# Optimization experiments

Measured on AMD Instinct MI355X. Metric: run time of the kernel, lower is better.

The kernel has to match this reference:

```python
import jax, jax.numpy as jnp
import numpy as np

NG, NU, NI, H = 5000, 100000, 20000, 128
E_UG, E_UI, E_GI = 300000, 600000, 200000


def setup_inputs() -> dict:
    key = jax.random.key(0)
    ks = jax.random.split(key, 20)
    s = 0.05  # weight scale for numeric stability
    inp = {
        'x_group': jnp.arange(NG, dtype=jnp.int64) if False else jnp.arange(NG),
        'x_user': jnp.arange(NU),
        'x_item': jnp.arange(NI),
        'emb_group': jax.random.normal(ks[0], (NG, H), jnp.float32) * s,
        'emb_user': jax.random.normal(ks[1], (NU, H), jnp.float32) * s,
        'emb_item': jax.random.normal(ks[2], (NI, H), jnp.float32) * s,
        'W1l': jax.random.normal(ks[3], (6, H, H), jnp.float32) * s,
        'W1r': jax.random.normal(ks[4], (6, H, H), jnp.float32) * s,
        'b1': jax.random.normal(ks[5], (6, H), jnp.float32) * s,
        'W2l': jax.random.normal(ks[6], (6, H, H), jnp.float32) * s,
        'W2r': jax.random.normal(ks[7], (6, H, H), jnp.float32) * s,
        'b2': jax.random.normal(ks[8], (6, H), jnp.float32) * s,
        'pred_W': jax.random.normal(ks[9], (H, NI), jnp.float32) * s,
        'pred_b': jax.random.normal(ks[10], (NI,), jnp.float32) * s,
        'ug_src': jax.random.randint(ks[11], (E_UG,), 0, NU),
        'ug_dst': jax.random.randint(ks[12], (E_UG,), 0, NG),
        'ui_src': jax.random.randint(ks[13], (E_UI,), 0, NU),
        'ui_dst': jax.random.randint(ks[14], (E_UI,), 0, NI),
        'gi_src': jax.random.randint(ks[15], (E_GI,), 0, NG),
        'gi_dst': jax.random.randint(ks[16], (E_GI,), 0, NI),
    }
    return inp


def _seg_mean(x, src, dst, n_dst):
    # gather neighbor features [E, H], scatter-sum to dst, divide by in-degree
    s = jax.ops.segment_sum(x[src], dst, num_segments=n_dst)
    cnt = jax.ops.segment_sum(jnp.ones(dst.shape[0], x.dtype), dst, num_segments=n_dst)
    return s / jnp.clip(cnt, 1.0)[:, None]


def _hetero_sage_layer(hg, hu, hi, Wl, Wr, b,
                       ug_src, ug_dst, ui_src, ui_dst, gi_src, gi_dst):
    # edge-type order: 0 u2g, 1 g2u, 2 u2i, 3 i2u, 4 g2i, 5 i2g
    ng, nu, ni = hg.shape[0], hu.shape[0], hi.shape[0]
    og = (_seg_mean(hu, ug_src, ug_dst, ng) @ Wl[0] + hg @ Wr[0] + b[0]
          + _seg_mean(hi, gi_dst, gi_src, ng) @ Wl[5] + hg @ Wr[5] + b[5])
    ou = (_seg_mean(hg, ug_dst, ug_src, nu) @ Wl[1] + hu @ Wr[1] + b[1]
          + _seg_mean(hi, ui_dst, ui_src, nu) @ Wl[3] + hu @ Wr[3] + b[3])
    oi = (_seg_mean(hu, ui_src, ui_dst, ni) @ Wl[2] + hi @ Wr[2] + b[2]
          + _seg_mean(hg, gi_src, gi_dst, ni) @ Wl[4] + hi @ Wr[4] + b[4])
    return og, ou, oi


def reference(x_group, x_user, x_item, emb_group, emb_user, emb_item,
              W1l, W1r, b1, W2l, W2r, b2, pred_W, pred_b,
              ug_src, ug_dst, ui_src, ui_dst, gi_src, gi_dst):
    # embedding lookup; group embeddings are zeroed in BaseGR.forward
    hg = emb_group[x_group] * 0.0
    hu = emb_user[x_user]
    hi = emb_item[x_item]
    og, ou, oi = _hetero_sage_layer(hg, hu, hi, W1l, W1r, b1,
                                    ug_src, ug_dst, ui_src, ui_dst, gi_src, gi_dst)
    hg, hu, hi = jax.nn.relu(og), jax.nn.relu(ou), jax.nn.relu(oi)
    og, ou, oi = _hetero_sage_layer(hg, hu, hi, W2l, W2r, b2,
                                    ug_src, ug_dst, ui_src, ui_dst, gi_src, gi_dst)
    rep_group = jax.nn.relu(og)
    # eval-mode output: group-level item scores [NG, NI]
    return rep_group @ pred_W + pred_b
```

## Files before the change

### kernel.cpp

```cpp
#include <hip/hip_runtime.h>

typedef __bf16 bf16x8 __attribute__((ext_vector_type(8)));
typedef __bf16 bf16x4 __attribute__((ext_vector_type(4)));
typedef __bf16 bf16x2 __attribute__((ext_vector_type(2)));
typedef float  f32x4  __attribute__((ext_vector_type(4)));

#define NG 5000
#define NU 100000
#define NI 20000
#define H  128
#define EUG 300000
#define EUI 600000
#define EGI 200000
#define ETOT (EUG + EGI + EUI + EUI)
#define NN  (2 * NG + NU + NI)

#define B_EMBU  0UL
#define B_EMBI  25600000UL
#define B_AGGU  30720000UL
#define B_AGGI  56320000UL
#define B_AGGG1 61440000UL
#define B_AGGG2 62720000UL
#define B_HG1   64000000UL
#define B_GU    65280000UL
#define B_GI    66560000UL
#define B_REP   67840000UL
#define B_BC    69120000UL
#define B_PWT   69122048UL
#define B_WT    74242048UL
#define B_CNT   74536960UL
#define B_OFFS  75056960UL
#define B_CUR   75576976UL
#define B_EIDX  76096976UL
#define B_EIT   82897024UL


#define SCAN_CHUNK 2048
#define NCHUNK 64

#define NB_PREP 10
#define NB_TP   626
#define NB_CVU  12500
#define NB_CVI  2500
#define NB_HIST 6641
#define NB_P1   (NB_PREP + NB_TP + NB_CVU + NB_CVI + NB_HIST)

#define NBU 782
#define NBI 157
#define NBG 40

__device__ __forceinline__ int swz(int row, int k) {
  return ((((k >> 3) ^ (row & 15)) << 3) | (k & 7));
}
__device__ __forceinline__ int cswz(int row, int col) {
  return col ^ (((row >> 2) & 1) << 4);
}

__device__ void prep_dev(const float* __restrict__ W1l, const float* __restrict__ W1r,
                         const float* __restrict__ W2l, const float* __restrict__ W2r,
                         const float* __restrict__ b1, const float* __restrict__ b2,
                         __bf16* __restrict__ WT, float* __restrict__ bc, int b, int tid) {
  if (b < 9) {
    const float* Wa; const float* Wb = nullptr;
    switch (b) {
      case 0: Wa = W1r + 1 * 16384; Wb = W1r + 3 * 16384; break;
      case 1: Wa = W1l + 3 * 16384; break;
      case 2: Wa = W1l + 2 * 16384; break;
      case 3: Wa = W1r + 2 * 16384; Wb = W1r + 4 * 16384; break;
      case 4: Wa = W1l + 0 * 16384; break;
      case 5: Wa = W1l + 5 * 16384; break;
      case 6: Wa = W2r + 0 * 16384; Wb = W2r + 5 * 16384; break;
      case 7: Wa = W2l + 0 * 16384; break;
      default: Wa = W2l + 5 * 16384; break;
    }
    __bf16* dst = WT + b * 16384;
    for (int idx = tid; idx < 16384; idx += 256) {
      int k = idx >> 7, c = idx & 127;
      float v = Wa[idx];
      if (Wb) v += Wb[idx];
      dst[c * 128 + k] = (__bf16)v;
    }
  } else {
    if (tid < 128) {
      bc[tid]       = b1[128 + tid]     + b1[3 * 128 + tid];
      bc[128 + tid] = b1[2 * 128 + tid] + b1[4 * 128 + tid];
      bc[256 + tid] = b1[tid]           + b1[5 * 128 + tid];
      bc[384 + tid] = b2[tid]           + b2[5 * 128 + tid];
    }
  }
}

__device__ void transpose_dev(const float* __restrict__ pw, __bf16* __restrict__ pwt,
                              int bx, int by, int tid, float (*t)[65]) {
  int i0 = bx * 64, k0 = by * 64;
  for (int idx = tid; idx < 64 * 16; idx += 256) {
    int kk = idx >> 4, c4 = (idx & 15) << 2;
    int ib = i0 + c4;
    float x0 = 0.f, x1 = 0.f, x2 = 0.f, x3 = 0.f;
    const float* src = pw + (size_t)(k0 + kk) * NI + ib;
    if (ib + 3 < NI) {
      const float4 v = *(const float4*)src;
      x0 = v.x; x1 = v.y; x2 = v.z; x3 = v.w;
    } else {
      if (ib + 0 < NI) x0 = src[0];
      if (ib + 1 < NI) x1 = src[1];
      if (ib + 2 < NI) x2 = src[2];
      if (ib + 3 < NI) x3 = src[3];
    }
    t[kk][c4 + 0] = x0; t[kk][c4 + 1] = x1; t[kk][c4 + 2] = x2; t[kk][c4 + 3] = x3;
  }
  __syncthreads();
  for (int idx = tid; idx < 64 * 16; idx += 256) {
    int ii = idx >> 4, k4 = (idx & 15) << 2;
    int gi = i0 + ii;
    if (gi < NI) {
      bf16x4 o;
      o[0] = (__bf16)t[k4 + 0][ii]; o[1] = (__bf16)t[k4 + 1][ii];
      o[2] = (__bf16)t[k4 + 2][ii]; o[3] = (__bf16)t[k4 + 3][ii];
      *(bf16x4*)(pwt + (size_t)gi * 128 + k0 + k4) = o;
    }
  }
}

__device__ void cvt_dev(const float* __restrict__ src, __bf16* __restrict__ dst,
                        int b, int tid, int n4) {
  int i = b * 256 + tid;
  if (i < n4) {
    float4 v = ((const float4*)src)[i];
    bf16x4 o;
    o[0] = (__bf16)v.x; o[1] = (__bf16)v.y; o[2] = (__bf16)v.z; o[3] = (__bf16)v.w;
    ((bf16x4*)dst)[i] = o;
  }
}

__device__ void hist_dev(const int* __restrict__ ug_dst, const int* __restrict__ gi_src,
                         const int* __restrict__ ui_src, const int* __restrict__ ui_dst,
                         int* __restrict__ cnt, int b, int tid) {
  int i = b * 256 + tid;
  int key, base;
  if (i < EUG)                       { key = ug_dst[i];                   base = 0; }
  else if (i < EUG + EGI)            { key = gi_src[i - EUG];             base = NG; }
  else if (i < EUG + EGI + EUI)      { key = ui_src[i - EUG - EGI];       base = 2 * NG; }
  else if (i < ETOT)                 { key = ui_dst[i - EUG - EGI - EUI]; base = 2 * NG + NU; }
  else return;
  atomicAdd(&cnt[base + key], 1);
}

__device__ void gemm_core(const __bf16* __restrict__ A0, const __bf16* __restrict__ B0,
                          const __bf16* __restrict__ A1, const __bf16* __restrict__ B1,
                          const __bf16* __restrict__ A2, const __bf16* __restrict__ B2,
                          const __bf16* __restrict__ Dadd, const float* __restrict__ bias,
                          float* __restrict__ Cf, __bf16* __restrict__ Cb,
                          int N, int NC, int nterms, int relu,
                          int rowblk, int colblk, char* smem_raw) {
  __bf16* sA = (__bf16*)smem_raw;
  __bf16* sB = sA + 128 * 128;
  float* sC = (float*)smem_raw;
  int tid = threadIdx.x;
  int rowbase = rowblk * 128, colbase = colblk * 128;
  int wid = tid >> 6, lane = tid & 63;
  int qrow = (wid >> 1) << 6, qcol = (wid & 1) << 6;
  int lrow = lane & 15, quad = lane >> 4;

  f32x4 acc[4][4];
#pragma unroll
  for (int mi = 0; mi < 4; ++mi)
#pragma unroll
    for (int ni = 0; ni < 4; ++ni) acc[mi][ni] = (f32x4){0.f, 0.f, 0.f, 0.f};

  const __bf16* As[3] = {A0, A1, A2};
  const __bf16* Bs[3] = {B0, B1, B2};

  for (int t = 0; t < nterms; ++t) {
    __syncthreads();
    const __bf16* A = As[t];
    for (int idx = tid; idx < 2048; idx += 256) {
      int row = idx >> 4, c8 = (idx & 15) << 3;
      int grow = rowbase + row;
      bf16x8 v;
      if (grow < N) v = *(const bf16x8*)(A + (size_t)grow * 128 + c8);
      else { for (int u = 0; u < 8; ++u) v[u] = (__bf16)0.f; }
      *(bf16x8*)&sA[row * 128 + swz(row, c8)] = v;
    }
    const __bf16* B = Bs[t];
    for (int idx = tid; idx < 2048; idx += 256) {
      int n = idx >> 4, c8 = (idx & 15) << 3;
      int gcol = colbase + n;
      bf16x8 v;
      if (gcol < NC) v = *(const bf16x8*)(B + (size_t)gcol * 128 + c8);
      else { for (int u = 0; u < 8; ++u) v[u] = (__bf16)0.f; }
      *(bf16x8*)&sB[n * 128 + swz(n, c8)] = v;
    }
    __syncthreads();
#pragma unroll
    for (int kb = 0; kb < 4; ++kb) {
      int k0 = kb * 32 + quad * 8;
      bf16x8 af[4], bfr[4];
#pragma unroll
      for (int mi = 0; mi < 4; ++mi) {
        int r = qrow + mi * 16 + lrow;
        af[mi] = *(const bf16x8*)&sA[r * 128 + swz(r, k0)];
      }
#pragma unroll
      for (int ni = 0; ni < 4; ++ni) {
        int r = qcol + ni * 16 + lrow;
        bfr[ni] = *(const bf16x8*)&sB[r * 128 + swz(r, k0)];
      }
#pragma unroll
      for (int mi = 0; mi < 4; ++mi)
#pragma unroll
        for (int ni = 0; ni < 4; ++ni)
          acc[mi][ni] = __builtin_amdgcn_mfma_f32_16x16x32_bf16(af[mi], bfr[ni], acc[mi][ni], 0, 0, 0);
    }
  }

  __syncthreads();
#pragma unroll
  for (int mi = 0; mi < 4; ++mi) {
#pragma unroll
    for (int ni = 0; ni < 4; ++ni) {
      int col = qcol + ni * 16 + lrow;
#pragma unroll
      for (int r = 0; r < 4; ++r) {
        int row = qrow + mi * 16 + quad * 4 + r;
        sC[row * 128 + cswz(row, col)] = acc[mi][ni][r];
      }
    }
  }
  __syncthreads();
  for (int idx = tid; idx < 4096; idx += 256) {
    int row = idx >> 5, c4 = (idx & 31) << 2;
    int grow = rowbase + row, gcol = colbase + c4;
    if (grow >= N) continue;
    f32x4 v = *(const f32x4*)&sC[row * 128 + cswz(row, c4)];
    if (gcol + 3 < NC) {
      if (bias) {
        f32x4 bv = *(const f32x4*)&bias[gcol];
        v += bv;
      }
      if (Dadd) {
        bf16x4 dv = *(const bf16x4*)(Dadd + (size_t)grow * 128 + gcol);
        v[0] += (float)dv[0]; v[1] += (float)dv[1];
        v[2] += (float)dv[2]; v[3] += (float)dv[3];
      }
      if (relu) {
#pragma unroll
        for (int u = 0; u < 4; ++u) v[u] = fmaxf(v[u], 0.f);
      }
      if (Cb) {
        bf16x4 o;
        o[0] = (__bf16)v[0]; o[1] = (__bf16)v[1]; o[2] = (__bf16)v[2]; o[3] = (__bf16)v[3];
        *(bf16x4*)(Cb + (size_t)grow * NC + gcol) = o;
      } else {
        __builtin_nontemporal_store(v, (f32x4*)(Cf + (size_t)grow * NC + gcol));
      }
    } else {
#pragma unroll
      for (int u = 0; u < 4; ++u) {
        if (gcol + u < NC) {
          float x = v[u] + (bias ? bias[gcol + u] : 0.f);
          if (Dadd) x += (float)Dadd[(size_t)grow * 128 + gcol + u];
          if (relu) x = fmaxf(x, 0.f);
          if (Cb) Cb[(size_t)grow * NC + gcol + u] = (__bf16)x;
          else    Cf[(size_t)grow * NC + gcol + u] = x;
        }
      }
    }
  }
}

__device__ void seg_dev(const __bf16* __restrict__ feat, const int* __restrict__ offs,
                        const int* __restrict__ eidx, __bf16* __restrict__ out,
                        int node, int orow, int lane) {
  int s = offs[node], e = offs[node + 1];
  float a0 = 0.f, a1 = 0.f;
  int j = s;
  for (; j + 4 <= e; j += 4) {
    int i0 = eidx[j], i1 = eidx[j + 1], i2 = eidx[j + 2], i3 = eidx[j + 3];
    bf16x2 v0 = *(const bf16x2*)(feat + (size_t)i0 * 128 + lane * 2);
    bf16x2 v1 = *(const bf16x2*)(feat + (size_t)i1 * 128 + lane * 2);
    bf16x2 v2 = *(const bf16x2*)(feat + (size_t)i2 * 128 + lane * 2);
    bf16x2 v3 = *(const bf16x2*)(feat + (size_t)i3 * 128 + lane * 2);
    a0 += (float)v0[0] + (float)v1[0] + (float)v2[0] + (float)v3[0];
    a1 += (float)v0[1] + (float)v1[1] + (float)v2[1] + (float)v3[1];
  }
  if (j + 2 <= e) {
    int i0 = eidx[j], i1 = eidx[j + 1];
    bf16x2 v0 = *(const bf16x2*)(feat + (size_t)i0 * 128 + lane * 2);
    bf16x2 v1 = *(const bf16x2*)(feat + (size_t)i1 * 128 + lane * 2);
    a0 += (float)v0[0] + (float)v1[0];
    a1 += (float)v0[1] + (float)v1[1];
    j += 2;
  }
  if (j < e) {
    int i0 = eidx[j];
    bf16x2 v0 = *(const bf16x2*)(feat + (size_t)i0 * 128 + lane * 2);
    a0 += (float)v0[0]; a1 += (float)v0[1];
  }
  float inv = (e > s) ? (1.f / (float)(e - s)) : 0.f;
  bf16x2 o;
  o[0] = (__bf16)(a0 * inv); o[1] = (__bf16)(a1 * inv);
  *(bf16x2*)(out + (size_t)orow * 128 + lane * 2) = o;
}

__global__ __launch_bounds__(256)
void phase1(const float* __restrict__ W1l, const float* __restrict__ W1r,
            const float* __restrict__ W2l, const float* __restrict__ W2r,
            const float* __restrict__ b1, const float* __restrict__ b2,
            const float* __restrict__ predW,
            const float* __restrict__ emb_user, const float* __restrict__ emb_item,
            const int* __restrict__ ug_dst, const int* __restrict__ gi_src,
            const int* __restrict__ ui_src, const int* __restrict__ ui_dst,
            char* __restrict__ ws) {
  __shared__ float tbuf[64][65];
  __bf16* WT = (__bf16*)(ws + B_WT);
  float* bc  = (float*)(ws + B_BC);
  __bf16* pwt = (__bf16*)(ws + B_PWT);
  __bf16* embU = (__bf16*)(ws + B_EMBU);
  __bf16* embI = (__bf16*)(ws + B_EMBI);
  int* cnt = (int*)(ws + B_CNT);
  int b = blockIdx.x, tid = threadIdx.x;
  if (b < NB_PREP) { prep_dev(W1l, W1r, W2l, W2r, b1, b2, WT, bc, b, tid); return; }
  b -= NB_PREP;
  if (b < NB_TP) { transpose_dev(predW, pwt, b % 313, b / 313, tid, tbuf); return; }
  b -= NB_TP;
  if (b < NB_CVU) { cvt_dev(emb_user, embU, b, tid, NU * 32); return; }
  b -= NB_CVU;
  if (b < NB_CVI) { cvt_dev(emb_item, embI, b, tid, NI * 32); return; }
  b -= NB_CVI;
  hist_dev(ug_dst, gi_src, ui_src, ui_dst, cnt, b, tid);
}

__global__ __launch_bounds__(256)
void scan_k1(const int* __restrict__ cnt, int* __restrict__ chunksum) {
  __shared__ int ws4[4];
  int b = blockIdx.x, tid = threadIdx.x, lane = tid & 63, w = tid >> 6;
  int base = b * SCAN_CHUNK + tid * 8;
  int s = 0;
#pragma unroll
  for (int j = 0; j < 8; ++j) { int i = base + j; if (i < NN) s += cnt[i]; }
#pragma unroll
  for (int d = 1; d < 64; d <<= 1) s += __shfl_xor(s, d, 64);
  if (lane == 0) ws4[w] = s;
  __syncthreads();
  if (tid == 0) chunksum[b] = ws4[0] + ws4[1] + ws4[2] + ws4[3];
}

__global__ __launch_bounds__(256)
void scan2_gemm0(char* __restrict__ ws) {
  __shared__ char smem[65536];
  int b = blockIdx.x, tid = threadIdx.x;
  if (b < NCHUNK) {
    int* shi = (int*)smem;
    const int* cnt = (const int*)(ws + B_CNT);
    const int* chunksum = (const int*)(ws + B_AGGU);
    int* offs = (int*)(ws + B_OFFS);
    int* cur  = (int*)(ws + B_CUR);
    int lane = tid & 63, w = tid >> 6;
    if (w == 0) {
      int v = chunksum[lane];
      int incl = v;
#pragma unroll
      for (int d = 1; d < 64; d <<= 1) { int t = __shfl_up(incl, d, 64); if (lane >= d) incl += t; }
      if (lane == b) shi[4] = incl - v;
    }
    int base = b * SCAN_CHUNK + tid * 8;
    int x[8]; int s = 0;
#pragma unroll
    for (int j = 0; j < 8; ++j) { int i = base + j; x[j] = (i < NN) ? cnt[i] : 0; s += x[j]; }
    int incl = s;
#pragma unroll
    for (int d = 1; d < 64; d <<= 1) { int t = __shfl_up(incl, d, 64); if (lane >= d) incl += t; }
    if (lane == 63) shi[w] = incl;
    __syncthreads();
    int wpre = 0;
    for (int ww = 0; ww < w; ++ww) wpre += shi[ww];
    int excl = shi[4] + wpre + incl - s;
#pragma unroll
    for (int j = 0; j < 8; ++j) {
      int i = base + j;
      if (i < NN) { offs[i] = excl; cur[i] = excl; }
      excl += x[j];
      if (i == NN - 1) offs[NN] = excl;
    }
  } else {
    const __bf16* embI = (const __bf16*)(ws + B_EMBI);
    const __bf16* WT   = (const __bf16*)(ws + B_WT);
    __bf16* eit = (__bf16*)(ws + B_EIT);
    gemm_core(embI, WT + 1 * 16384, nullptr, nullptr, nullptr, nullptr,
              nullptr, nullptr, nullptr, eit, NI, 128, 1, 0, b - NCHUNK, 0, smem);
  }
}

__global__ __launch_bounds__(256)
void fill_all(const int* __restrict__ ug_src, const int* __restrict__ ug_dst,
              const int* __restrict__ gi_src, const int* __restrict__ gi_dst,
              const int* __restrict__ ui_src, const int* __restrict__ ui_dst,
              int* __restrict__ cur, int* __restrict__ eidx) {
  int i = blockIdx.x * 256 + threadIdx.x;
  int key, base, payload;
  if (i < EUG)                  { key = ug_dst[i];       base = 0;            payload = ug_src[i]; }
  else if (i < EUG + EGI)       { int j = i - EUG;       key = gi_src[j]; base = NG;          payload = gi_dst[j]; }
  else if (i < EUG + EGI + EUI) { int j = i - EUG - EGI; key = ui_src[j]; base = 2 * NG;      payload = ui_dst[j]; }
  else if (i < ETOT)            { int j = i - EUG - EGI - EUI; key = ui_dst[j]; base = 2 * NG + NU; payload = ui_src[j]; }
  else return;
  int pos = atomicAdd(&cur[base + key], 1);
  eidx[pos] = payload;
}

__global__ __launch_bounds__(256)
void seg1(char* __restrict__ ws) {
  int w = threadIdx.x >> 6, lane = threadIdx.x & 63;
  int node = blockIdx.x * 4 + w;
  if (node >= NN) return;
  const int* offs = (const int*)(ws + B_OFFS);
  const int* eidx = (const int*)(ws + B_EIDX);
  const __bf16* feat; __bf16* out; int orow;
  if (node < NG)               { feat = (const __bf16*)(ws + B_EMBU); out = (__bf16*)(ws + B_AGGG1); orow = node; }
  else if (node < 2 * NG)      { feat = (const __bf16*)(ws + B_EMBI); out = (__bf16*)(ws + B_AGGG2); orow = node - NG; }
  else if (node < 2 * NG + NU) { feat = (const __bf16*)(ws + B_EIT);  out = (__bf16*)(ws + B_AGGU);  orow = node - 2 * NG; }
  else                         { feat = (const __bf16*)(ws + B_EMBU); out = (__bf16*)(ws + B_AGGI);  orow = node - 2 * NG - NU; }
  seg_dev(feat, offs, eidx, out, node, orow, lane);
}

__global__ __launch_bounds__(256)
void gemm1(char* __restrict__ ws) {
  __shared__ char smem[65536];
  const __bf16* WT = (const __bf16*)(ws + B_WT);
  const float* bc  = (const float*)(ws + B_BC);
  int b = blockIdx.x;
  if (b < NBU) {
    __bf16* aggU = (__bf16*)(ws + B_AGGU);
    gemm_core((const __bf16*)(ws + B_EMBU), WT + 0 * 16384,
              nullptr, nullptr, nullptr, nullptr,
              aggU, bc + 0, nullptr, aggU, NU, 128, 1, 1, b, 0, smem);
  } else if (b < NBU + NBI) {
    __bf16* aggI = (__bf16*)(ws + B_AGGI);
    gemm_core(aggI, WT + 2 * 16384,
              (const __bf16*)(ws + B_EMBI), WT + 3 * 16384, nullptr, nullptr,
              nullptr, bc + 128, nullptr, aggI, NI, 128, 2, 1, b - NBU, 0, smem);
  } else {
    gemm_core((const __bf16*)(ws + B_AGGG1), WT + 4 * 16384,
              (const __bf16*)(ws + B_AGGG2), WT + 5 * 16384, nullptr, nullptr,
              nullptr, bc + 256, nullptr, (__bf16*)(ws + B_HG1), NG, 128, 2, 1,
              b - NBU - NBI, 0, smem);
  }
}

__global__ __launch_bounds__(256)
void seg2(char* __restrict__ ws) {
  int w = threadIdx.x >> 6, lane = threadIdx.x & 63;
  int node = blockIdx.x * 4 + w;
  if (node >= 2 * NG) return;
  const int* offs = (const int*)(ws + B_OFFS);
  const int* eidx = (const int*)(ws + B_EIDX);
  const __bf16* feat; __bf16* out; int orow;
  if (node < NG) { feat = (const __bf16*)(ws + B_AGGU); out = (__bf16*)(ws + B_GU); orow = node; }
  else           { feat = (const __bf16*)(ws + B_AGGI); out = (__bf16*)(ws + B_GI); orow = node - NG; }
  seg_dev(feat, offs, eidx, out, node, orow, lane);
}

__global__ __launch_bounds__(256)
void gemm2(char* __restrict__ ws) {
  __shared__ char smem[65536];
  const __bf16* WT = (const __bf16*)(ws + B_WT);
  const float* bc  = (const float*)(ws + B_BC);
  gemm_core((const __bf16*)(ws + B_GU),  WT + 7 * 16384,
            (const __bf16*)(ws + B_HG1), WT + 6 * 16384,
            (const __bf16*)(ws + B_GI),  WT + 8 * 16384,
            nullptr, bc + 384, nullptr, (__bf16*)(ws + B_REP), NG, 128, 3, 1,
            blockIdx.x, 0, smem);
}

__global__ __launch_bounds__(256)
void gemmF(char* __restrict__ ws, const float* __restrict__ predb, float* __restrict__ out) {
  __shared__ char smem[65536];
  gemm_core((const __bf16*)(ws + B_REP), (const __bf16*)(ws + B_PWT),
            nullptr, nullptr, nullptr, nullptr,
            nullptr, predb, out, nullptr, NG, NI, 1, 0,
            blockIdx.x, blockIdx.y, smem);
}

extern "C" void kernel_launch(void* const* d_in, const int* in_sizes, int n_in,
                              void* d_out, int out_size, void* d_ws, size_t ws_size,
                              hipStream_t stream) {
  const float* emb_user = (const float*)d_in[4];
  const float* emb_item = (const float*)d_in[5];
  const float* W1l = (const float*)d_in[6];
  const float* W1r = (const float*)d_in[7];
  const float* b1  = (const float*)d_in[8];
  const float* W2l = (const float*)d_in[9];
  const float* W2r = (const float*)d_in[10];
  const float* b2  = (const float*)d_in[11];
  const float* predW = (const float*)d_in[12];
  const float* predb = (const float*)d_in[13];
  const int* ug_src = (const int*)d_in[14];
  const int* ug_dst = (const int*)d_in[15];
  const int* ui_src = (const int*)d_in[16];
  const int* ui_dst = (const int*)d_in[17];
  const int* gi_src = (const int*)d_in[18];
  const int* gi_dst = (const int*)d_in[19];

  char* ws = (char*)d_ws;
  int* cnt  = (int*)(ws + B_CNT);
  int* cur  = (int*)(ws + B_CUR);
  int* eidx = (int*)(ws + B_EIDX);
  int* chunksum = (int*)(ws + B_AGGU);

  hipMemsetAsync(cnt, 0, NN * sizeof(int), stream);

  phase1<<<NB_P1, 256, 0, stream>>>(W1l, W1r, W2l, W2r, b1, b2, predW,
                                    emb_user, emb_item,
                                    ug_dst, gi_src, ui_src, ui_dst, ws);
  scan_k1<<<NCHUNK, 256, 0, stream>>>(cnt, chunksum);
  scan2_gemm0<<<NCHUNK + NBI, 256, 0, stream>>>(ws);
  fill_all<<<(ETOT + 255) / 256, 256, 0, stream>>>(ug_src, ug_dst, gi_src, gi_dst,
                                                   ui_src, ui_dst, cur, eidx);
  seg1<<<(NN + 3) / 4, 256, 0, stream>>>(ws);
  gemm1<<<NBU + NBI + NBG, 256, 0, stream>>>(ws);
  seg2<<<(2 * NG + 3) / 4, 256, 0, stream>>>(ws);
  gemm2<<<NBG, 256, 0, stream>>>(ws);
  gemmF<<<dim3(NBG, NBI), 256, 0, stream>>>(ws, predb, (float*)d_out);
}
```

Measured before the change: 924.5 us.

## Merge pipeline into two persistent kernels with software grid barriers

Replaces nine kernel launches with two persistent kernels (768 and 384 blocks) that loop over virtual blocks and synchronise between phases with an atomic generation-counter grid barrier. The algebra is also reordered: the item-to-user transform is no longer precomputed before aggregation but applied afterwards in the user GEMM as a second term, which drops the EIT buffer and the Dadd epilogue. The segment-mean routine is changed so each half-wave handles alternate edges with 4-wide loads and a shuffle reduce. This removes launch gaps and the pre-GEMM, but the barriers assume all blocks are co-resident, give up on a timeout, and persistent grids may balance work less well.

```diff
diff --git a/kernel.cpp b/kernel.cpp
--- a/kernel.cpp
+++ b/kernel.cpp
@@ -28,11 +28,11 @@
 #define B_BC    69120000UL
 #define B_PWT   69122048UL
 #define B_WT    74242048UL
-#define B_CNT   74536960UL
-#define B_OFFS  75056960UL
-#define B_CUR   75576976UL
-#define B_EIDX  76096976UL
-#define B_EIT   82897024UL
+#define B_BAR   74536960UL
+#define B_CNT   74537088UL
+#define B_OFFS  75057088UL
+#define B_CUR   75577104UL
+#define B_EIDX  76097104UL
 
 
 #define SCAN_CHUNK 2048
@@ -48,6 +48,29 @@
 #define NBU 782
 #define NBI 157
 #define NBG 40
+
+#define GRID_B 768
+#define GRID_C 384
+
+__device__ __forceinline__ void gbar(int* bar, int nb) {
+  __syncthreads();
+  if (threadIdx.x == 0) {
+    int* cnt = bar;
+    int* gen = bar + 16;
+    int g = __hip_atomic_load(gen, __ATOMIC_RELAXED, __HIP_MEMORY_SCOPE_AGENT);
+    if (__hip_atomic_fetch_add(cnt, 1, __ATOMIC_ACQ_REL, __HIP_MEMORY_SCOPE_AGENT) == nb - 1) {
+      __hip_atomic_store(cnt, 0, __ATOMIC_RELAXED, __HIP_MEMORY_SCOPE_AGENT);
+      __hip_atomic_store(gen, g + 1, __ATOMIC_RELEASE, __HIP_MEMORY_SCOPE_AGENT);
+    } else {
+      int spins = 0;
+      while (__hip_atomic_load(gen, __ATOMIC_ACQUIRE, __HIP_MEMORY_SCOPE_AGENT) == g) {
+        __builtin_amdgcn_s_sleep(8);
+        if (++spins > (1 << 16)) break;
+      }
+    }
+  }
+  __syncthreads();
+}
 
 __device__ __forceinline__ int swz(int row, int k) {
   return ((((k >> 3) ^ (row & 15)) << 3) | (k & 7));
@@ -120,6 +143,7 @@
       *(bf16x4*)(pwt + (size_t)gi * 128 + k0 + k4) = o;
     }
   }
+  __syncthreads();
 }
 
 __device__ void cvt_dev(const float* __restrict__ src, __bf16* __restrict__ dst,
@@ -149,7 +173,7 @@
 __device__ void gemm_core(const __bf16* __restrict__ A0, const __bf16* __restrict__ B0,
                           const __bf16* __restrict__ A1, const __bf16* __restrict__ B1,
                           const __bf16* __restrict__ A2, const __bf16* __restrict__ B2,
-                          const __bf16* __restrict__ Dadd, const float* __restrict__ bias,
+                          const float* __restrict__ bias,
                           float* __restrict__ Cf, __bf16* __restrict__ Cb,
                           int N, int NC, int nterms, int relu,
                           int rowblk, int colblk, char* smem_raw) {
@@ -238,11 +262,6 @@
         f32x4 bv = *(const f32x4*)&bias[gcol];
         v += bv;
       }
-      if (Dadd) {
-        bf16x4 dv = *(const bf16x4*)(Dadd + (size_t)grow * 128 + gcol);
-        v[0] += (float)dv[0]; v[1] += (float)dv[1];
-        v[2] += (float)dv[2]; v[3] += (float)dv[3];
-      }
       if (relu) {
 #pragma unroll
         for (int u = 0; u < 4; ++u) v[u] = fmaxf(v[u], 0.f);
@@ -259,7 +278,6 @@
       for (int u = 0; u < 4; ++u) {
         if (gcol + u < NC) {
           float x = v[u] + (bias ? bias[gcol + u] : 0.f);
-          if (Dadd) x += (float)Dadd[(size_t)grow * 128 + gcol + u];
           if (relu) x = fmaxf(x, 0.f);
           if (Cb) Cb[(size_t)grow * NC + gcol + u] = (__bf16)x;
           else    Cf[(size_t)grow * NC + gcol + u] = x;
@@ -267,104 +285,110 @@
       }
     }
   }
+  __syncthreads();
 }
 
 __device__ void seg_dev(const __bf16* __restrict__ feat, const int* __restrict__ offs,
                         const int* __restrict__ eidx, __bf16* __restrict__ out,
                         int node, int orow, int lane) {
   int s = offs[node], e = offs[node + 1];
-  float a0 = 0.f, a1 = 0.f;
-  int j = s;
-  for (; j + 4 <= e; j += 4) {
-    int i0 = eidx[j], i1 = eidx[j + 1], i2 = eidx[j + 2], i3 = eidx[j + 3];
-    bf16x2 v0 = *(const bf16x2*)(feat + (size_t)i0 * 128 + lane * 2);
-    bf16x2 v1 = *(const bf16x2*)(feat + (size_t)i1 * 128 + lane * 2);
-    bf16x2 v2 = *(const bf16x2*)(feat + (size_t)i2 * 128 + lane * 2);
-    bf16x2 v3 = *(const bf16x2*)(feat + (size_t)i3 * 128 + lane * 2);
-    a0 += (float)v0[0] + (float)v1[0] + (float)v2[0] + (float)v3[0];
-    a1 += (float)v0[1] + (float)v1[1] + (float)v2[1] + (float)v3[1];
-  }
-  if (j + 2 <= e) {
-    int i0 = eidx[j], i1 = eidx[j + 1];
-    bf16x2 v0 = *(const bf16x2*)(feat + (size_t)i0 * 128 + lane * 2);
-    bf16x2 v1 = *(const bf16x2*)(feat + (size_t)i1 * 128 + lane * 2);
+  int half = lane >> 5;
+  int l4 = (lane & 31) << 2;
+  float a0 = 0.f, a1 = 0.f, a2 = 0.f, a3 = 0.f;
+  int j = s + half;
+  for (; j + 2 < e; j += 4) {
+    int r0 = eidx[j], r1 = eidx[j + 2];
+    bf16x4 v0 = *(const bf16x4*)(feat + (size_t)r0 * 128 + l4);
+    bf16x4 v1 = *(const bf16x4*)(feat + (size_t)r1 * 128 + l4);
     a0 += (float)v0[0] + (float)v1[0];
     a1 += (float)v0[1] + (float)v1[1];
-    j += 2;
+    a2 += (float)v0[2] + (float)v1[2];
+    a3 += (float)v0[3] + (float)v1[3];
   }
   if (j < e) {
-    int i0 = eidx[j];
-    bf16x2 v0 = *(const bf16x2*)(feat + (size_t)i0 * 128 + lane * 2);
-    a0 += (float)v0[0]; a1 += (float)v0[1];
-  }
-  float inv = (e > s) ? (1.f / (float)(e - s)) : 0.f;
-  bf16x2 o;
-  o[0] = (__bf16)(a0 * inv); o[1] = (__bf16)(a1 * inv);
-  *(bf16x2*)(out + (size_t)orow * 128 + lane * 2) = o;
-}
-
-__global__ __launch_bounds__(256)
-void phase1(const float* __restrict__ W1l, const float* __restrict__ W1r,
-            const float* __restrict__ W2l, const float* __restrict__ W2r,
-            const float* __restrict__ b1, const float* __restrict__ b2,
-            const float* __restrict__ predW,
-            const float* __restrict__ emb_user, const float* __restrict__ emb_item,
-            const int* __restrict__ ug_dst, const int* __restrict__ gi_src,
-            const int* __restrict__ ui_src, const int* __restrict__ ui_dst,
-            char* __restrict__ ws) {
+    int r0 = eidx[j];
+    bf16x4 v0 = *(const bf16x4*)(feat + (size_t)r0 * 128 + l4);
+    a0 += (float)v0[0]; a1 += (float)v0[1]; a2 += (float)v0[2]; a3 += (float)v0[3];
+  }
+  a0 += __shfl_xor(a0, 32, 64);
+  a1 += __shfl_xor(a1, 32, 64);
+  a2 += __shfl_xor(a2, 32, 64);
+  a3 += __shfl_xor(a3, 32, 64);
+  if (half == 0) {
+    float inv = (e > s) ? (1.f / (float)(e - s)) : 0.f;
+    bf16x4 o;
+    o[0] = (__bf16)(a0 * inv); o[1] = (__bf16)(a1 * inv);
+    o[2] = (__bf16)(a2 * inv); o[3] = (__bf16)(a3 * inv);
+    *(bf16x4*)(out + (size_t)orow * 128 + l4) = o;
+  }
+}
+
+__global__ __launch_bounds__(256, 4)
+void coopB(const float* __restrict__ W1l, const float* __restrict__ W1r,
+           const float* __restrict__ W2l, const float* __restrict__ W2r,
+           const float* __restrict__ b1, const float* __restrict__ b2,
+           const float* __restrict__ predW,
+           const float* __restrict__ emb_user, const float* __restrict__ emb_item,
+           const int* __restrict__ ug_src, const int* __restrict__ ug_dst,
+           const int* __restrict__ ui_src, const int* __restrict__ ui_dst,
+           const int* __restrict__ gi_src, const int* __restrict__ gi_dst,
+           char* __restrict__ ws) {
   __shared__ float tbuf[64][65];
+  __shared__ int shi[8];
+  int tid = threadIdx.x;
+  int nb = gridDim.x;
+  int* bar = (int*)(ws + B_BAR);
+
   __bf16* WT = (__bf16*)(ws + B_WT);
   float* bc  = (float*)(ws + B_BC);
   __bf16* pwt = (__bf16*)(ws + B_PWT);
   __bf16* embU = (__bf16*)(ws + B_EMBU);
   __bf16* embI = (__bf16*)(ws + B_EMBI);
-  int* cnt = (int*)(ws + B_CNT);
-  int b = blockIdx.x, tid = threadIdx.x;
-  if (b < NB_PREP) { prep_dev(W1l, W1r, W2l, W2r, b1, b2, WT, bc, b, tid); return; }
-  b -= NB_PREP;
-  if (b < NB_TP) { transpose_dev(predW, pwt, b % 313, b / 313, tid, tbuf); return; }
-  b -= NB_TP;
-  if (b < NB_CVU) { cvt_dev(emb_user, embU, b, tid, NU * 32); return; }
-  b -= NB_CVU;
-  if (b < NB_CVI) { cvt_dev(emb_item, embI, b, tid, NI * 32); return; }
-  b -= NB_CVI;
-  hist_dev(ug_dst, gi_src, ui_src, ui_dst, cnt, b, tid);
-}
-
-__global__ __launch_bounds__(256)
-void scan_k1(const int* __restrict__ cnt, int* __restrict__ chunksum) {
-  __shared__ int ws4[4];
-  int b = blockIdx.x, tid = threadIdx.x, lane = tid & 63, w = tid >> 6;
-  int base = b * SCAN_CHUNK + tid * 8;
-  int s = 0;
-#pragma unroll
-  for (int j = 0; j < 8; ++j) { int i = base + j; if (i < NN) s += cnt[i]; }
-#pragma unroll
-  for (int d = 1; d < 64; d <<= 1) s += __shfl_xor(s, d, 64);
-  if (lane == 0) ws4[w] = s;
-  __syncthreads();
-  if (tid == 0) chunksum[b] = ws4[0] + ws4[1] + ws4[2] + ws4[3];
-}
-
-__global__ __launch_bounds__(256)
-void scan2_gemm0(char* __restrict__ ws) {
-  __shared__ char smem[65536];
-  int b = blockIdx.x, tid = threadIdx.x;
-  if (b < NCHUNK) {
-    int* shi = (int*)smem;
-    const int* cnt = (const int*)(ws + B_CNT);
-    const int* chunksum = (const int*)(ws + B_AGGU);
-    int* offs = (int*)(ws + B_OFFS);
-    int* cur  = (int*)(ws + B_CUR);
+  int* cnt  = (int*)(ws + B_CNT);
+  int* offs = (int*)(ws + B_OFFS);
+  int* cur  = (int*)(ws + B_CUR);
+  int* eidx = (int*)(ws + B_EIDX);
+  int* chunksum = (int*)(ws + B_AGGU);
+
+  for (int vb = blockIdx.x; vb < NB_P1; vb += nb) {
+    int b = vb;
+    if (b < NB_PREP) { prep_dev(W1l, W1r, W2l, W2r, b1, b2, WT, bc, b, tid); continue; }
+    b -= NB_PREP;
+    if (b < NB_TP) { transpose_dev(predW, pwt, b % 313, b / 313, tid, tbuf); continue; }
+    b -= NB_TP;
+    if (b < NB_CVU) { cvt_dev(emb_user, embU, b, tid, NU * 32); continue; }
+    b -= NB_CVU;
+    if (b < NB_CVI) { cvt_dev(emb_item, embI, b, tid, NI * 32); continue; }
+    b -= NB_CVI;
+    hist_dev(ug_dst, gi_src, ui_src, ui_dst, cnt, b, tid);
+  }
+  gbar(bar, nb);
+
+  for (int vb = blockIdx.x; vb < NCHUNK; vb += nb) {
+    int lane = tid & 63, w = tid >> 6;
+    int base = vb * SCAN_CHUNK + tid * 8;
+    int s = 0;
+#pragma unroll
+    for (int j = 0; j < 8; ++j) { int i = base + j; if (i < NN) s += cnt[i]; }
+#pragma unroll
+    for (int d = 1; d < 64; d <<= 1) s += __shfl_xor(s, d, 64);
+    if (lane == 0) shi[w] = s;
+    __syncthreads();
+    if (tid == 0) chunksum[vb] = shi[0] + shi[1] + shi[2] + shi[3];
+    __syncthreads();
+  }
+  gbar(bar, nb);
+
+  for (int vb = blockIdx.x; vb < NCHUNK; vb += nb) {
     int lane = tid & 63, w = tid >> 6;
     if (w == 0) {
       int v = chunksum[lane];
       int incl = v;
 #pragma unroll
       for (int d = 1; d < 64; d <<= 1) { int t = __shfl_up(incl, d, 64); if (lane >= d) incl += t; }
-      if (lane == b) shi[4] = incl - v;
-    }
-    int base = b * SCAN_CHUNK + tid * 8;
+      if (lane == vb) shi[4] = incl - v;
+    }
+    int base = vb * SCAN_CHUNK + tid * 8;
     int x[8]; int s = 0;
 #pragma unroll
     for (int j = 0; j < 8; ++j) { int i = base + j; x[j] = (i < NN) ? cnt[i] : 0; s += x[j]; }
@@ -383,102 +407,97 @@
       excl += x[j];
       if (i == NN - 1) offs[NN] = excl;
     }
-  } else {
-    const __bf16* embI = (const __bf16*)(ws + B_EMBI);
-    const __bf16* WT   = (const __bf16*)(ws + B_WT);
-    __bf16* eit = (__bf16*)(ws + B_EIT);
-    gemm_core(embI, WT + 1 * 16384, nullptr, nullptr, nullptr, nullptr,
-              nullptr, nullptr, nullptr, eit, NI, 128, 1, 0, b - NCHUNK, 0, smem);
-  }
-}
-
-__global__ __launch_bounds__(256)
-void fill_all(const int* __restrict__ ug_src, const int* __restrict__ ug_dst,
-              const int* __restrict__ gi_src, const int* __restrict__ gi_dst,
-              const int* __restrict__ ui_src, const int* __restrict__ ui_dst,
-              int* __restrict__ cur, int* __restrict__ eidx) {
-  int i = blockIdx.x * 256 + threadIdx.x;
-  int key, base, payload;
-  if (i < EUG)                  { key = ug_dst[i];       base = 0;            payload = ug_src[i]; }
-  else if (i < EUG + EGI)       { int j = i - EUG;       key = gi_src[j]; base = NG;          payload = gi_dst[j]; }
-  else if (i < EUG + EGI + EUI) { int j = i - EUG - EGI; key = ui_src[j]; base = 2 * NG;      payload = ui_dst[j]; }
-  else if (i < ETOT)            { int j = i - EUG - EGI - EUI; key = ui_dst[j]; base = 2 * NG + NU; payload = ui_src[j]; }
-  else return;
-  int pos = atomicAdd(&cur[base + key], 1);
-  eidx[pos] = payload;
-}
-
-__global__ __launch_bounds__(256)
-void seg1(char* __restrict__ ws) {
-  int w = threadIdx.x >> 6, lane = threadIdx.x & 63;
-  int node = blockIdx.x * 4 + w;
-  if (node >= NN) return;
+    __syncthreads();
+  }
+  gbar(bar, nb);
+
+  for (int i = blockIdx.x * 256 + tid; i < ETOT; i += nb * 256) {
+    int key, base, payload;
+    if (i < EUG)                  { key = ug_dst[i];       base = 0;            payload = ug_src[i]; }
+    else if (i < EUG + EGI)       { int j = i - EUG;       key = gi_src[j]; base = NG;          payload = gi_dst[j]; }
+    else if (i < EUG + EGI + EUI) { int j = i - EUG - EGI; key = ui_src[j]; base = 2 * NG;      payload = ui_dst[j]; }
+    else                          { int j = i - EUG - EGI - EUI; key = ui_dst[j]; base = 2 * NG + NU; payload = ui_src[j]; }
+    int pos = atomicAdd(&cur[base + key], 1);
+    eidx[pos] = payload;
+  }
+  gbar(bar, nb);
+
+  {
+    int w = tid >> 6, lane = tid & 63;
+    __bf16* aggU = (__bf16*)(ws + B_AGGU);
+    __bf16* aggI = (__bf16*)(ws + B_AGGI);
+    __bf16* aggG1 = (__bf16*)(ws + B_AGGG1);
+    __bf16* aggG2 = (__bf16*)(ws + B_AGGG2);
+    for (int node = blockIdx.x * 4 + w; node < NN; node += nb * 4) {
+      const __bf16* feat; __bf16* out; int orow;
+      if (node < NG)               { feat = embU; out = aggG1; orow = node; }
+      else if (node < 2 * NG)      { feat = embI; out = aggG2; orow = node - NG; }
+      else if (node < 2 * NG + NU) { feat = embI; out = aggU;  orow = node - 2 * NG; }
+      else                         { feat = embU; out = aggI;  orow = node - 2 * NG - NU; }
+      seg_dev(feat, offs, eidx, out, node, orow, lane);
+    }
+  }
+}
+
+__global__ __launch_bounds__(256, 2)
+void coopC(char* __restrict__ ws, const float* __restrict__ predb,
+           float* __restrict__ out) {
+  __shared__ char smem[65536];
+  int nb = gridDim.x;
+  int* bar = (int*)(ws + B_BAR);
+
+  const __bf16* WT = (const __bf16*)(ws + B_WT);
+  const float* bc  = (const float*)(ws + B_BC);
   const int* offs = (const int*)(ws + B_OFFS);
   const int* eidx = (const int*)(ws + B_EIDX);
-  const __bf16* feat; __bf16* out; int orow;
-  if (node < NG)               { feat = (const __bf16*)(ws + B_EMBU); out = (__bf16*)(ws + B_AGGG1); orow = node; }
-  else if (node < 2 * NG)      { feat = (const __bf16*)(ws + B_EMBI); out = (__bf16*)(ws + B_AGGG2); orow = node - NG; }
-  else if (node < 2 * NG + NU) { feat = (const __bf16*)(ws + B_EIT);  out = (__bf16*)(ws + B_AGGU);  orow = node - 2 * NG; }
-  else                         { feat = (const __bf16*)(ws + B_EMBU); out = (__bf16*)(ws + B_AGGI);  orow = node - 2 * NG - NU; }
-  seg_dev(feat, offs, eidx, out, node, orow, lane);
-}
-
-__global__ __launch_bounds__(256)
-void gemm1(char* __restrict__ ws) {
-  __shared__ char smem[65536];
-  const __bf16* WT = (const __bf16*)(ws + B_WT);
-  const float* bc  = (const float*)(ws + B_BC);
-  int b = blockIdx.x;
-  if (b < NBU) {
-    __bf16* aggU = (__bf16*)(ws + B_AGGU);
-    gemm_core((const __bf16*)(ws + B_EMBU), WT + 0 * 16384,
-              nullptr, nullptr, nullptr, nullptr,
-              aggU, bc + 0, nullptr, aggU, NU, 128, 1, 1, b, 0, smem);
-  } else if (b < NBU + NBI) {
-    __bf16* aggI = (__bf16*)(ws + B_AGGI);
-    gemm_core(aggI, WT + 2 * 16384,
-              (const __bf16*)(ws + B_EMBI), WT + 3 * 16384, nullptr, nullptr,
-              nullptr, bc + 128, nullptr, aggI, NI, 128, 2, 1, b - NBU, 0, smem);
-  } else {
-    gemm_core((const __bf16*)(ws + B_AGGG1), WT + 4 * 16384,
-              (const __bf16*)(ws + B_AGGG2), WT + 5 * 16384, nullptr, nullptr,
-              nullptr, bc + 256, nullptr, (__bf16*)(ws + B_HG1), NG, 128, 2, 1,
-              b - NBU - NBI, 0, smem);
-  }
-}
-
-__global__ __launch_bounds__(256)
-void seg2(char* __restrict__ ws) {
-  int w = threadIdx.x >> 6, lane = threadIdx.x & 63;
-  int node = blockIdx.x * 4 + w;
-  if (node >= 2 * NG) return;
-  const int* offs = (const int*)(ws + B_OFFS);
-  const int* eidx = (const int*)(ws + B_EIDX);
-  const __bf16* feat; __bf16* out; int orow;
-  if (node < NG) { feat = (const __bf16*)(ws + B_AGGU); out = (__bf16*)(ws + B_GU); orow = node; }
-  else           { feat = (const __bf16*)(ws + B_AGGI); out = (__bf16*)(ws + B_GI); orow = node - NG; }
-  seg_dev(feat, offs, eidx, out, node, orow, lane);
-}
-
-__global__ __launch_bounds__(256)
-void gemm2(char* __restrict__ ws) {
-  __shared__ char smem[65536];
-  const __bf16* WT = (const __bf16*)(ws + B_WT);
-  const float* bc  = (const float*)(ws + B_BC);
-  gemm_core((const __bf16*)(ws + B_GU),  WT + 7 * 16384,
-            (const __bf16*)(ws + B_HG1), WT + 6 * 16384,
-            (const __bf16*)(ws + B_GI),  WT + 8 * 16384,
-            nullptr, bc + 384, nullptr, (__bf16*)(ws + B_REP), NG, 128, 3, 1,
-            blockIdx.x, 0, smem);
-}
-
-__global__ __launch_bounds__(256)
-void gemmF(char* __restrict__ ws, const float* __restrict__ predb, float* __restrict__ out) {
-  __shared__ char smem[65536];
-  gemm_core((const __bf16*)(ws + B_REP), (const __bf16*)(ws + B_PWT),
-            nullptr, nullptr, nullptr, nullptr,
-            nullptr, predb, out, nullptr, NG, NI, 1, 0,
-            blockIdx.x, blockIdx.y, smem);
+  __bf16* embU = (__bf16*)(ws + B_EMBU);
+  __bf16* embI = (__bf16*)(ws + B_EMBI);
+  __bf16* aggU = (__bf16*)(ws + B_AGGU);
+  __bf16* aggI = (__bf16*)(ws + B_AGGI);
+  __bf16* aggG1 = (__bf16*)(ws + B_AGGG1);
+  __bf16* aggG2 = (__bf16*)(ws + B_AGGG2);
+  __bf16* hg1 = (__bf16*)(ws + B_HG1);
+  __bf16* gU  = (__bf16*)(ws + B_GU);
+  __bf16* gI  = (__bf16*)(ws + B_GI);
+  __bf16* rep = (__bf16*)(ws + B_REP);
+  const __bf16* pwt = (const __bf16*)(ws + B_PWT);
+
+  for (int vb = blockIdx.x; vb < NBU + NBI + NBG; vb += nb) {
+    if (vb < NBU) {
+      gemm_core(embU, WT + 0 * 16384, aggU, WT + 1 * 16384, nullptr, nullptr,
+                bc + 0, nullptr, aggU, NU, 128, 2, 1, vb, 0, smem);
+    } else if (vb < NBU + NBI) {
+      gemm_core(aggI, WT + 2 * 16384, embI, WT + 3 * 16384, nullptr, nullptr,
+                bc + 128, nullptr, aggI, NI, 128, 2, 1, vb - NBU, 0, smem);
+    } else {
+      gemm_core(aggG1, WT + 4 * 16384, aggG2, WT + 5 * 16384, nullptr, nullptr,
+                bc + 256, nullptr, hg1, NG, 128, 2, 1, vb - NBU - NBI, 0, smem);
+    }
+  }
+  gbar(bar, nb);
+
+  {
+    int w = threadIdx.x >> 6, lane = threadIdx.x & 63;
+    for (int node = blockIdx.x * 4 + w; node < 2 * NG; node += nb * 4) {
+      const __bf16* feat; __bf16* outp; int orow;
+      if (node < NG) { feat = aggU; outp = gU; orow = node; }
+      else           { feat = aggI; outp = gI; orow = node - NG; }
+      seg_dev(feat, offs, eidx, outp, node, orow, lane);
+    }
+  }
+  gbar(bar, nb);
+
+  for (int vb = blockIdx.x; vb < NBG; vb += nb) {
+    gemm_core(gU, WT + 7 * 16384, hg1, WT + 6 * 16384, gI, WT + 8 * 16384,
+              bc + 384, nullptr, rep, NG, 128, 3, 1, vb, 0, smem);
+  }
+  gbar(bar, nb);
+
+  for (int vb = blockIdx.x; vb < NBG * NBI; vb += nb) {
+    int rb = vb / NBI, cb = vb % NBI;
+    gemm_core(rep, pwt, nullptr, nullptr, nullptr, nullptr,
+              predb, out, nullptr, NG, NI, 1, 0, rb, cb, smem);
+  }
 }
 
 extern "C" void kernel_launch(void* const* d_in, const int* in_sizes, int n_in,
@@ -502,23 +521,12 @@
   const int* gi_dst = (const int*)d_in[19];
 
   char* ws = (char*)d_ws;
-  int* cnt  = (int*)(ws + B_CNT);
-  int* cur  = (int*)(ws + B_CUR);
-  int* eidx = (int*)(ws + B_EIDX);
-  int* chunksum = (int*)(ws + B_AGGU);
-
-  hipMemsetAsync(cnt, 0, NN * sizeof(int), stream);
-
-  phase1<<<NB_P1, 256, 0, stream>>>(W1l, W1r, W2l, W2r, b1, b2, predW,
+
+  hipMemsetAsync(ws + B_BAR, 0, 128 + NN * sizeof(int), stream);
+
+  coopB<<<GRID_B, 256, 0, stream>>>(W1l, W1r, W2l, W2r, b1, b2, predW,
                                     emb_user, emb_item,
-                                    ug_dst, gi_src, ui_src, ui_dst, ws);
-  scan_k1<<<NCHUNK, 256, 0, stream>>>(cnt, chunksum);
-  scan2_gemm0<<<NCHUNK + NBI, 256, 0, stream>>>(ws);
-  fill_all<<<(ETOT + 255) / 256, 256, 0, stream>>>(ug_src, ug_dst, gi_src, gi_dst,
-                                                   ui_src, ui_dst, cur, eidx);
-  seg1<<<(NN + 3) / 4, 256, 0, stream>>>(ws);
-  gemm1<<<NBU + NBI + NBG, 256, 0, stream>>>(ws);
-  seg2<<<(2 * NG + 3) / 4, 256, 0, stream>>>(ws);
-  gemm2<<<NBG, 256, 0, stream>>>(ws);
-  gemmF<<<dim3(NBG, NBI), 256, 0, stream>>>(ws, predb, (float*)d_out);
-}
+                                    ug_src, ug_dst, ui_src, ui_dst,
+                                    gi_src, gi_dst, ws);
+  coopC<<<GRID_C, 256, 0, stream>>>(ws, predb, (float*)d_out);
+}
```

New measurement: 1.988 ms. +115.1%, slower.
